# Kernel optimization log

Measured on AMD Instinct MI355X. Metric: run time of the kernel, lower is better.

Reference implementation:

```python
import jax, jax.numpy as jnp
import numpy as np

CHNN = 1024
K = 2048


def _conv1x1(W, b, x):
    # x: (B, C_in, L), W: (C_out, C_in), b: (C_out,)
    return jnp.einsum('oc,bcl->bol', W, x) + b[None, :, None]


def setup_inputs() -> dict:
    key = jax.random.key(0)
    ks = jax.random.split(key, 10)
    s = 0.02
    return {
        'vc': jax.random.normal(ks[0], (1, CHNN, K), dtype=jnp.float32),
        'vm': jax.random.normal(ks[1], (1, CHNN, K), dtype=jnp.float32),
        'W_ak': jax.random.normal(ks[2], (K, CHNN), dtype=jnp.float32) * s,
        'b_ak': jax.random.normal(ks[3], (K,), dtype=jnp.float32) * s,
        'W_c': jax.random.normal(ks[4], (CHNN, CHNN), dtype=jnp.float32) * s,
        'b_c': jax.random.normal(ks[5], (CHNN,), dtype=jnp.float32) * s,
        'W_mad': jax.random.normal(ks[6], (CHNN, CHNN), dtype=jnp.float32) * s,
        'b_mad': jax.random.normal(ks[7], (CHNN,), dtype=jnp.float32) * s,
        'W_gcn': jax.random.normal(ks[8], (CHNN, CHNN), dtype=jnp.float32) * s,
        'b_gcn': jax.random.normal(ks[9], (CHNN,), dtype=jnp.float32) * s,
    }


def reference(vc, vm, W_ak, b_ak, W_c, b_c, W_mad, b_mad, W_gcn, b_gcn):
    # vcw: (1, K, L) assignment logits; softmax over the K (channel) dim
    vcw = _conv1x1(W_ak, b_ak, vc)
    vcw = jax.nn.softmax(vcw, axis=1)
    w = vcw[0].T                      # (L, K)  (batch forced to 1 by squeeze(0))
    # vm features: (1, CHNN, K)
    vmr = jax.nn.relu(_conv1x1(W_c, b_c, vm))
    # F.linear(vm, w): contract last dim (K) with w's second dim -> (1, CHNN, L)
    vma = jnp.einsum('bck,lk->bcl', vmr, w)
    vma = _conv1x1(W_mad, b_mad, vma)  # (1, CHNN, L)
    # dense adjacency over positions: (1, L, L)
    A = jnp.einsum('bck,bcl->bkl', vma, vma)
    # GCN: x (1, K, CHNN) @ W + b, then softmax(A) @ x  (requires L == K)
    x = jnp.swapaxes(vmr, 1, 2) @ W_gcn + b_gcn
    A = jax.nn.softmax(A, axis=-1)
    out = A @ x                        # (1, L, CHNN)
    return jnp.swapaxes(out, 1, 2)     # (1, CHNN, L)
```

## Files before the change

### kernel.cpp

```cpp
#include <hip/hip_runtime.h>
#include <hip/hip_bf16.h>


typedef __bf16 bf16x4 __attribute__((ext_vector_type(4)));
typedef __bf16 bf16x8 __attribute__((ext_vector_type(8)));
typedef float  f32x4  __attribute__((ext_vector_type(4)));

typedef const void __attribute__((address_space(1)))* gptr_t;
typedef void       __attribute__((address_space(3)))* lptr_t;

__device__ __forceinline__ void load16_lds(const __bf16* g, __bf16* l)
{
    __builtin_amdgcn_global_load_lds((gptr_t)g, (lptr_t)l, 16, 0, 0);
}

template<typename OT, int TM_, int TN_, int BIAS_, bool RELU_, int STORE_>
struct GC {
    using OUT_T = OT;
    static constexpr int TM = TM_, TN = TN_, BIAS = BIAS_, STORE = STORE_;
    static constexpr bool RELU = RELU_;
    static constexpr int SMEM = 2 * (TM_ + TN_) * 32 * 2;
};

template<class CF>
__device__ __forceinline__ void gemm_body(
    int bid, char* smem,
    const __bf16* __restrict__ A, const __bf16* __restrict__ B,
    const float* __restrict__ bias,
    typename CF::OUT_T* __restrict__ C, typename CF::OUT_T* __restrict__ CT,
    int M, int N, int K, int ntx)
{
    constexpr int TM = CF::TM, TN = CF::TN;
    constexpr int FM = TM / 32, FN = TN / 32;
    constexpr int NA = TM / 64, NB = TN / 64;
    __bf16* sA = (__bf16*)smem;
    __bf16* sB = (__bf16*)smem + 2 * TM * 32;
    const int tid = threadIdx.x, lane = tid & 63, wv = tid >> 6;
    const int m0 = (bid / ntx) * TM, n0 = (bid % ntx) * TN;
    const int mw = (wv >> 1) * (FM * 16), nw = (wv & 1) * (FN * 16);

    f32x4 acc[FM][FN];
    #pragma unroll
    for (int i = 0; i < FM; ++i)
        #pragma unroll
        for (int j = 0; j < FN; ++j)
            acc[i][j] = (f32x4){0.f, 0.f, 0.f, 0.f};

    const __bf16* gA = A + (size_t)m0 * K;
    const __bf16* gB = B + (size_t)n0 * K;

    auto stage = [&](int k0, int buf) {
        #pragma unroll
        for (int i = 0; i < NA; ++i) {
            const int c = (wv * NA + i) * 64 + lane;
            load16_lds(gA + (size_t)(c >> 2) * K + k0 + (c & 3) * 8,
                       &sA[buf * TM * 32 + (wv * NA + i) * 512]);
        }
        #pragma unroll
        for (int i = 0; i < NB; ++i) {
            const int c = (wv * NB + i) * 64 + lane;
            load16_lds(gB + (size_t)(c >> 2) * K + k0 + (c & 3) * 8,
                       &sB[buf * TN * 32 + (wv * NB + i) * 512]);
        }
    };

    stage(0, 0);
    int cur = 0;
    for (int k0 = 0; k0 < K; k0 += 32) {
        __syncthreads();
        if (k0 + 32 < K) stage(k0 + 32, cur ^ 1);
        bf16x8 af[FM], bfr[FN];
        #pragma unroll
        for (int i = 0; i < FM; ++i)
            af[i] = *(const bf16x8*)&sA[cur * TM * 32 + (mw + i * 16 + (lane & 15)) * 32 + (lane >> 4) * 8];
        #pragma unroll
        for (int j = 0; j < FN; ++j)
            bfr[j] = *(const bf16x8*)&sB[cur * TN * 32 + (nw + j * 16 + (lane & 15)) * 32 + (lane >> 4) * 8];
        #pragma unroll
        for (int i = 0; i < FM; ++i)
            #pragma unroll
            for (int j = 0; j < FN; ++j)
                acc[i][j] = __builtin_amdgcn_mfma_f32_16x16x32_bf16(af[i], bfr[j], acc[i][j], 0, 0, 0);
        cur ^= 1;
    }

    #pragma unroll
    for (int i = 0; i < FM; ++i) {
        const int rowb = m0 + mw + i * 16 + (lane >> 4) * 4;
        #pragma unroll
        for (int j = 0; j < FN; ++j) {
            const int col = n0 + nw + j * 16 + (lane & 15);
            f32x4 v = acc[i][j];
            #pragma unroll
            for (int r = 0; r < 4; ++r) {
                float f = v[r];
                if (CF::BIAS == 1) f += bias[rowb + r];
                if (CF::BIAS == 2) f += bias[col];
                if (CF::RELU) f = fmaxf(f, 0.f);
                v[r] = f;
            }
            if (CF::STORE == 0 || CF::STORE == 2) {
                #pragma unroll
                for (int r = 0; r < 4; ++r)
                    C[(size_t)(rowb + r) * N + col] = (typename CF::OUT_T)v[r];
            }
            if (CF::STORE == 1 || CF::STORE == 2) {
                if constexpr (sizeof(typename CF::OUT_T) == 4) {
                    *(f32x4*)&CT[(size_t)col * M + rowb] = v;
                } else {
                    bf16x4 w = { (__bf16)v[0], (__bf16)v[1], (__bf16)v[2], (__bf16)v[3] };
                    *(bf16x4*)&CT[(size_t)col * M + rowb] = w;
                }
            }
        }
    }
}

template<class CF>
__global__ __launch_bounds__(256, 2)
void gemm1(const __bf16* __restrict__ A, const __bf16* __restrict__ B,
           const float* __restrict__ bias,
           typename CF::OUT_T* __restrict__ C, typename CF::OUT_T* __restrict__ CT,
           int M, int N, int K, int ntx)
{
    __shared__ char smem[CF::SMEM];
    gemm_body<CF>(blockIdx.x, smem, A, B, bias, C, CT, M, N, K, ntx);
}

template<class C1, class C2>
__global__ __launch_bounds__(256, 2)
void gemm2(int nblk1,
           const __bf16* __restrict__ A1, const __bf16* __restrict__ B1,
           const float* __restrict__ b1,
           typename C1::OUT_T* __restrict__ C1p, typename C1::OUT_T* __restrict__ CT1,
           int M1, int N1, int K1, int ntx1,
           const __bf16* __restrict__ A2, const __bf16* __restrict__ B2,
           const float* __restrict__ b2,
           typename C2::OUT_T* __restrict__ C2p, typename C2::OUT_T* __restrict__ CT2,
           int M2, int N2, int K2, int ntx2)
{
    constexpr int S = C1::SMEM > C2::SMEM ? C1::SMEM : C2::SMEM;
    __shared__ char smem[S];
    if ((int)blockIdx.x < nblk1)
        gemm_body<C1>(blockIdx.x, smem, A1, B1, b1, C1p, CT1, M1, N1, K1, ntx1);
    else
        gemm_body<C2>(blockIdx.x - nblk1, smem, A2, B2, b2, C2p, CT2, M2, N2, K2, ntx2);
}

__device__ __forceinline__ void softmax_row(__bf16* __restrict__ p)
{
    __shared__ float red[256];
    const int t = threadIdx.x;
    bf16x8 v = *(bf16x8*)&p[t * 8];
    float f[8];
    float m = -1e30f;
    #pragma unroll
    for (int r = 0; r < 8; ++r) { f[r] = (float)v[r]; m = fmaxf(m, f[r]); }
    red[t] = m;
    __syncthreads();
    for (int s = 128; s > 0; s >>= 1) {
        if (t < s) red[t] = fmaxf(red[t], red[t + s]);
        __syncthreads();
    }
    m = red[0];
    __syncthreads();
    float sum = 0.f;
    #pragma unroll
    for (int r = 0; r < 8; ++r) { f[r] = expf(f[r] - m); sum += f[r]; }
    red[t] = sum;
    __syncthreads();
    for (int s = 128; s > 0; s >>= 1) {
        if (t < s) red[t] += red[t + s];
        __syncthreads();
    }
    const float inv = 1.f / red[0];
    bf16x8 w;
    #pragma unroll
    for (int r = 0; r < 8; ++r) w[r] = (__bf16)(f[r] * inv);
    *(bf16x8*)&p[t * 8] = w;
}

template<class C1, class C2>
__global__ __launch_bounds__(256, 2)
void gemm2sm(int nblk1, int nblk2,
             const __bf16* __restrict__ A1, const __bf16* __restrict__ B1,
             const float* __restrict__ b1,
             typename C1::OUT_T* __restrict__ C1p,
             int M1, int N1, int K1, int ntx1,
             const __bf16* __restrict__ A2, const __bf16* __restrict__ B2,
             const float* __restrict__ b2,
             typename C2::OUT_T* __restrict__ C2p,
             int M2, int N2, int K2, int ntx2,
             __bf16* __restrict__ SM)
{
    constexpr int S = C1::SMEM > C2::SMEM ? C1::SMEM : C2::SMEM;
    __shared__ char smem[S];
    const int b = blockIdx.x;
    if (b < nblk1)
        gemm_body<C1>(b, smem, A1, B1, b1, C1p, (typename C1::OUT_T*)nullptr,
                      M1, N1, K1, ntx1);
    else if (b < nblk1 + nblk2)
        gemm_body<C2>(b - nblk1, smem, A2, B2, b2, C2p, (typename C2::OUT_T*)nullptr,
                      M2, N2, K2, ntx2);
    else
        softmax_row(SM + (size_t)(b - nblk1 - nblk2) * 2048);
}

__device__ __forceinline__ void tp_tile(const float* __restrict__ in,
                                        __bf16* __restrict__ outp,
                                        int R, int C, int bx, int by)
{
    __shared__ float t[32][33];
    const int tx = threadIdx.x & 31, ty = threadIdx.x >> 5;
    #pragma unroll
    for (int i = ty; i < 32; i += 8)
        t[i][tx] = in[(size_t)(by + i) * C + (bx + tx)];
    __syncthreads();
    #pragma unroll
    for (int i = ty; i < 32; i += 8)
        outp[(size_t)(bx + i) * R + (by + tx)] = (__bf16)t[tx][i];
}

__device__ __forceinline__ void cast_blk(const float* __restrict__ s,
                                         __bf16* __restrict__ d, int blk)
{
    const int i = blk * 1024 + threadIdx.x * 4;
    float4 v = *(const float4*)&s[i];
    bf16x4 w = { (__bf16)v.x, (__bf16)v.y, (__bf16)v.z, (__bf16)v.w };
    *(bf16x4*)&d[i] = w;
}

__global__ __launch_bounds__(256)
void prep(const float* __restrict__ vc, __bf16* __restrict__ vcT,
          const float* __restrict__ vm, __bf16* __restrict__ vmT,
          const float* __restrict__ W_ak, __bf16* __restrict__ W_akb,
          const float* __restrict__ W_c, __bf16* __restrict__ W_cb,
          const float* __restrict__ W_mad, __bf16* __restrict__ W_madb,
          const float* __restrict__ W_gcn, __bf16* __restrict__ W_gcnT)
{
    const int x = blockIdx.x;
    if (blockIdx.z == 0) {
        const float* in = (x < 2048) ? vc : vm;
        __bf16* o       = (x < 2048) ? vcT : vmT;
        const int e = x & 2047;
        tp_tile(in, o, 1024, 2048, (e & 63) * 32, (e >> 6) * 32);
    } else if (blockIdx.z == 1) {
        if (x < 2048)      cast_blk(W_ak, W_akb, x);
        else if (x < 3072) cast_blk(W_c, W_cb, x - 2048);
        else               cast_blk(W_mad, W_madb, x - 3072);
    } else {
        if (x >= 1024) return;
        tp_tile(W_gcn, W_gcnT, 1024, 1024, (x & 31) * 32, (x >> 5) * 32);
    }
}

__global__ __launch_bounds__(256)
void row_softmax_k(__bf16* __restrict__ A)
{
    softmax_row(A + (size_t)blockIdx.x * 2048);
}

extern "C" void kernel_launch(void* const* d_in, const int* in_sizes, int n_in,
                              void* d_out, int out_size, void* d_ws, size_t ws_size,
                              hipStream_t stream)
{
    const float* vc    = (const float*)d_in[0];
    const float* vm    = (const float*)d_in[1];
    const float* W_ak  = (const float*)d_in[2];
    const float* b_ak  = (const float*)d_in[3];
    const float* W_c   = (const float*)d_in[4];
    const float* b_c   = (const float*)d_in[5];
    const float* W_mad = (const float*)d_in[6];
    const float* b_mad = (const float*)d_in[7];
    const float* W_gcn = (const float*)d_in[8];
    const float* b_gcn = (const float*)d_in[9];
    float* out = (float*)d_out;

    char* ws = (char*)d_ws;
    const size_t MB = 1u << 20;
    __bf16* ST     = (__bf16*)(ws);
    __bf16* P      = (__bf16*)(ws);
    __bf16* vcT    = (__bf16*)(ws + 8 * MB);
    __bf16* vmaT   = (__bf16*)(ws + 8 * MB);
    __bf16* W_akb  = (__bf16*)(ws + 12 * MB);
    __bf16* vmm    = (__bf16*)(ws + 12 * MB);
    __bf16* vmT    = (__bf16*)(ws + 16 * MB);
    __bf16* xT     = (__bf16*)(ws + 16 * MB);
    __bf16* W_cb   = (__bf16*)(ws + 20 * MB);
    __bf16* W_madb = (__bf16*)(ws + 22 * MB);
    __bf16* vmrT   = (__bf16*)(ws + 24 * MB);
    __bf16* W_gcnT = (__bf16*)(ws + 28 * MB);

    using G3  = GC<__bf16, 128, 64, 2, false, 0>;
    using G5  = GC<__bf16, 128, 64, 1, true,  1>;
    using G6  = GC<__bf16, 128, 64, 0, false, 0>;
    using G11 = GC<__bf16, 128, 64, 1, false, 0>;
    using G7  = GC<__bf16, 64,  64, 2, false, 0>;
    using G9  = GC<__bf16, 128, 64, 0, false, 0>;
    using G12 = GC<float,  64,  64, 0, false, 1>;

    prep<<<dim3(4096, 1, 3), 256, 0, stream>>>(vc, vcT, vm, vmT, W_ak, W_akb,
                                               W_c, W_cb, W_mad, W_madb,
                                               W_gcn, W_gcnT);
    gemm2<G3, G5><<<768, 256, 0, stream>>>(512,
        vcT, W_akb, b_ak, ST, (__bf16*)nullptr, 2048, 2048, 1024, 32,
        W_cb, vmT, b_c, (__bf16*)nullptr, vmrT, 1024, 2048, 1024, 32);
    gemm2sm<G6, G11><<<2560, 256, 0, stream>>>(256, 256,
        W_madb, vmrT, nullptr, vmm, 1024, 2048, 1024, 32,
        W_gcnT, vmrT, b_gcn, xT, 1024, 2048, 1024, 32,
        ST);
    gemm1<G7><<<512, 256, 0, stream>>>(ST, vmm, b_mad, vmaT, (__bf16*)nullptr,
                                       2048, 1024, 2048, 16);
    gemm1<G9><<<512, 256, 0, stream>>>(vmaT, vmaT, nullptr, P, (__bf16*)nullptr,
                                       2048, 2048, 1024, 32);
    row_softmax_k<<<2048, 256, 0, stream>>>(P);
    gemm1<G12><<<512, 256, 0, stream>>>(P, xT, nullptr, (float*)nullptr, out,
                                        2048, 1024, 2048, 16);
}
```

Baseline: 211.3 us.

## Switch GEMMs and softmax to single-wave blocks with barrier-free waitcnt pipelining

Reworks every GEMM into a 64-thread block that owns a 64x64 tile. Because there is only one wave, __syncthreads is replaced by s_waitcnt on vmcnt, and the direct-to-LDS loads are double-buffered with a prefetch distance of two stages. Row softmax is rewritten to use one wave and shuffle reductions, removing the LDS tree reduction and barriers. The cost is more blocks, less operand reuse across waves, and reliance on hand-coded waitcnt encodings being correct for LDS-bound async loads.

Result: no change. 208.2 us (-1.4%).

```diff
diff --git a/kernel.cpp b/kernel.cpp
--- a/kernel.cpp
+++ b/kernel.cpp
@@ -14,82 +14,91 @@
     __builtin_amdgcn_global_load_lds((gptr_t)g, (lptr_t)l, 16, 0, 0);
 }
 
-template<typename OT, int TM_, int TN_, int BIAS_, bool RELU_, int STORE_>
+#define WAITCNT_VM8 0x0F78
+#define WAITCNT_VM0 0x0F70
+
+template<typename OT, int BIAS_, bool RELU_, int STORE_>
 struct GC {
     using OUT_T = OT;
-    static constexpr int TM = TM_, TN = TN_, BIAS = BIAS_, STORE = STORE_;
+    static constexpr int BIAS = BIAS_, STORE = STORE_;
     static constexpr bool RELU = RELU_;
-    static constexpr int SMEM = 2 * (TM_ + TN_) * 32 * 2;
 };
 
 template<class CF>
 __device__ __forceinline__ void gemm_body(
-    int bid, char* smem,
+    int bid, __bf16* sA, __bf16* sB,
     const __bf16* __restrict__ A, const __bf16* __restrict__ B,
     const float* __restrict__ bias,
     typename CF::OUT_T* __restrict__ C, typename CF::OUT_T* __restrict__ CT,
     int M, int N, int K, int ntx)
 {
-    constexpr int TM = CF::TM, TN = CF::TN;
-    constexpr int FM = TM / 32, FN = TN / 32;
-    constexpr int NA = TM / 64, NB = TN / 64;
-    __bf16* sA = (__bf16*)smem;
-    __bf16* sB = (__bf16*)smem + 2 * TM * 32;
-    const int tid = threadIdx.x, lane = tid & 63, wv = tid >> 6;
-    const int m0 = (bid / ntx) * TM, n0 = (bid % ntx) * TN;
-    const int mw = (wv >> 1) * (FM * 16), nw = (wv & 1) * (FN * 16);
-
-    f32x4 acc[FM][FN];
-    #pragma unroll
-    for (int i = 0; i < FM; ++i)
-        #pragma unroll
-        for (int j = 0; j < FN; ++j)
-            acc[i][j] = (f32x4){0.f, 0.f, 0.f, 0.f};
-
+    const int lane = threadIdx.x & 63;
+    const int m0 = (bid / ntx) * 64, n0 = (bid % ntx) * 64;
     const __bf16* gA = A + (size_t)m0 * K;
     const __bf16* gB = B + (size_t)n0 * K;
 
+    f32x4 acc[4][4];
+    #pragma unroll
+    for (int i = 0; i < 4; ++i)
+        #pragma unroll
+        for (int j = 0; j < 4; ++j)
+            acc[i][j] = (f32x4){0.f, 0.f, 0.f, 0.f};
+
     auto stage = [&](int k0, int buf) {
         #pragma unroll
-        for (int i = 0; i < NA; ++i) {
-            const int c = (wv * NA + i) * 64 + lane;
+        for (int i = 0; i < 4; ++i) {
+            const int c = i * 64 + lane;
             load16_lds(gA + (size_t)(c >> 2) * K + k0 + (c & 3) * 8,
-                       &sA[buf * TM * 32 + (wv * NA + i) * 512]);
-        }
-        #pragma unroll
-        for (int i = 0; i < NB; ++i) {
-            const int c = (wv * NB + i) * 64 + lane;
+                       &sA[buf * 2048 + i * 512]);
+        }
+        #pragma unroll
+        for (int i = 0; i < 4; ++i) {
+            const int c = i * 64 + lane;
             load16_lds(gB + (size_t)(c >> 2) * K + k0 + (c & 3) * 8,
-                       &sB[buf * TN * 32 + (wv * NB + i) * 512]);
+                       &sB[buf * 2048 + i * 512]);
         }
     };
 
     stage(0, 0);
+    stage(32, 1);
     int cur = 0;
-    for (int k0 = 0; k0 < K; k0 += 32) {
-        __syncthreads();
-        if (k0 + 32 < K) stage(k0 + 32, cur ^ 1);
-        bf16x8 af[FM], bfr[FN];
-        #pragma unroll
-        for (int i = 0; i < FM; ++i)
-            af[i] = *(const bf16x8*)&sA[cur * TM * 32 + (mw + i * 16 + (lane & 15)) * 32 + (lane >> 4) * 8];
-        #pragma unroll
-        for (int j = 0; j < FN; ++j)
-            bfr[j] = *(const bf16x8*)&sB[cur * TN * 32 + (nw + j * 16 + (lane & 15)) * 32 + (lane >> 4) * 8];
-        #pragma unroll
-        for (int i = 0; i < FM; ++i)
+    for (int k0 = 0; k0 < K - 32; k0 += 32) {
+        __builtin_amdgcn_s_waitcnt(WAITCNT_VM8);
+        bf16x8 af[4], bfr[4];
+        #pragma unroll
+        for (int i = 0; i < 4; ++i) {
+            af[i]  = *(const bf16x8*)&sA[cur * 2048 + (i * 16 + (lane & 15)) * 32 + (lane >> 4) * 8];
+            bfr[i] = *(const bf16x8*)&sB[cur * 2048 + (i * 16 + (lane & 15)) * 32 + (lane >> 4) * 8];
+        }
+        #pragma unroll
+        for (int i = 0; i < 4; ++i)
             #pragma unroll
-            for (int j = 0; j < FN; ++j)
+            for (int j = 0; j < 4; ++j)
                 acc[i][j] = __builtin_amdgcn_mfma_f32_16x16x32_bf16(af[i], bfr[j], acc[i][j], 0, 0, 0);
+        if (k0 + 64 < K) stage(k0 + 64, cur);
         cur ^= 1;
     }
-
-    #pragma unroll
-    for (int i = 0; i < FM; ++i) {
-        const int rowb = m0 + mw + i * 16 + (lane >> 4) * 4;
-        #pragma unroll
-        for (int j = 0; j < FN; ++j) {
-            const int col = n0 + nw + j * 16 + (lane & 15);
+    __builtin_amdgcn_s_waitcnt(WAITCNT_VM0);
+    {
+        bf16x8 af[4], bfr[4];
+        #pragma unroll
+        for (int i = 0; i < 4; ++i) {
+            af[i]  = *(const bf16x8*)&sA[cur * 2048 + (i * 16 + (lane & 15)) * 32 + (lane >> 4) * 8];
+            bfr[i] = *(const bf16x8*)&sB[cur * 2048 + (i * 16 + (lane & 15)) * 32 + (lane >> 4) * 8];
+        }
+        #pragma unroll
+        for (int i = 0; i < 4; ++i)
+            #pragma unroll
+            for (int j = 0; j < 4; ++j)
+                acc[i][j] = __builtin_amdgcn_mfma_f32_16x16x32_bf16(af[i], bfr[j], acc[i][j], 0, 0, 0);
+    }
+
+    #pragma unroll
+    for (int i = 0; i < 4; ++i) {
+        const int rowb = m0 + i * 16 + (lane >> 4) * 4;
+        #pragma unroll
+        for (int j = 0; j < 4; ++j) {
+            const int col = n0 + j * 16 + (lane & 15);
             f32x4 v = acc[i][j];
             #pragma unroll
             for (int r = 0; r < 4; ++r) {
@@ -99,12 +108,11 @@
                 if (CF::RELU) f = fmaxf(f, 0.f);
                 v[r] = f;
             }
-            if (CF::STORE == 0 || CF::STORE == 2) {
+            if (CF::STORE == 0) {
                 #pragma unroll
                 for (int r = 0; r < 4; ++r)
                     C[(size_t)(rowb + r) * N + col] = (typename CF::OUT_T)v[r];
-            }
-            if (CF::STORE == 1 || CF::STORE == 2) {
+            } else {
                 if constexpr (sizeof(typename CF::OUT_T) == 4) {
                     *(f32x4*)&CT[(size_t)col * M + rowb] = v;
                 } else {
@@ -116,94 +124,97 @@
     }
 }
 
+__device__ __forceinline__ void softmax_row_w(__bf16* __restrict__ p)
+{
+    const int lane = threadIdx.x & 63;
+    bf16x8 v[4];
+    float f[32];
+    #pragma unroll
+    for (int r = 0; r < 4; ++r)
+        v[r] = *(const bf16x8*)&p[(r * 64 + lane) * 8];
+    float m = -1e30f;
+    #pragma unroll
+    for (int r = 0; r < 4; ++r)
+        #pragma unroll
+        for (int j = 0; j < 8; ++j) {
+            f[r * 8 + j] = (float)v[r][j];
+            m = fmaxf(m, f[r * 8 + j]);
+        }
+    #pragma unroll
+    for (int s = 1; s < 64; s <<= 1) m = fmaxf(m, __shfl_xor(m, s, 64));
+    float sum = 0.f;
+    #pragma unroll
+    for (int i = 0; i < 32; ++i) { f[i] = expf(f[i] - m); sum += f[i]; }
+    #pragma unroll
+    for (int s = 1; s < 64; s <<= 1) sum += __shfl_xor(sum, s, 64);
+    const float inv = 1.f / sum;
+    #pragma unroll
+    for (int r = 0; r < 4; ++r) {
+        bf16x8 w;
+        #pragma unroll
+        for (int j = 0; j < 8; ++j) w[j] = (__bf16)(f[r * 8 + j] * inv);
+        *(bf16x8*)&p[(r * 64 + lane) * 8] = w;
+    }
+}
+
 template<class CF>
-__global__ __launch_bounds__(256, 2)
-void gemm1(const __bf16* __restrict__ A, const __bf16* __restrict__ B,
-           const float* __restrict__ bias,
-           typename CF::OUT_T* __restrict__ C, typename CF::OUT_T* __restrict__ CT,
-           int M, int N, int K, int ntx)
-{
-    __shared__ char smem[CF::SMEM];
-    gemm_body<CF>(blockIdx.x, smem, A, B, bias, C, CT, M, N, K, ntx);
+__global__ __launch_bounds__(64, 2)
+void gemm1w(const __bf16* __restrict__ A, const __bf16* __restrict__ B,
+            const float* __restrict__ bias,
+            typename CF::OUT_T* __restrict__ C, typename CF::OUT_T* __restrict__ CT,
+            int M, int N, int K, int ntx)
+{
+    __shared__ __bf16 sAB[8192];
+    gemm_body<CF>(blockIdx.x, sAB, sAB + 4096, A, B, bias, C, CT, M, N, K, ntx);
 }
 
 template<class C1, class C2>
-__global__ __launch_bounds__(256, 2)
-void gemm2(int nblk1,
-           const __bf16* __restrict__ A1, const __bf16* __restrict__ B1,
-           const float* __restrict__ b1,
-           typename C1::OUT_T* __restrict__ C1p, typename C1::OUT_T* __restrict__ CT1,
-           int M1, int N1, int K1, int ntx1,
-           const __bf16* __restrict__ A2, const __bf16* __restrict__ B2,
-           const float* __restrict__ b2,
-           typename C2::OUT_T* __restrict__ C2p, typename C2::OUT_T* __restrict__ CT2,
-           int M2, int N2, int K2, int ntx2)
-{
-    constexpr int S = C1::SMEM > C2::SMEM ? C1::SMEM : C2::SMEM;
-    __shared__ char smem[S];
-    if ((int)blockIdx.x < nblk1)
-        gemm_body<C1>(blockIdx.x, smem, A1, B1, b1, C1p, CT1, M1, N1, K1, ntx1);
-    else
-        gemm_body<C2>(blockIdx.x - nblk1, smem, A2, B2, b2, C2p, CT2, M2, N2, K2, ntx2);
-}
-
-__device__ __forceinline__ void softmax_row(__bf16* __restrict__ p)
-{
-    __shared__ float red[256];
-    const int t = threadIdx.x;
-    bf16x8 v = *(bf16x8*)&p[t * 8];
-    float f[8];
-    float m = -1e30f;
-    #pragma unroll
-    for (int r = 0; r < 8; ++r) { f[r] = (float)v[r]; m = fmaxf(m, f[r]); }
-    red[t] = m;
-    __syncthreads();
-    for (int s = 128; s > 0; s >>= 1) {
-        if (t < s) red[t] = fmaxf(red[t], red[t + s]);
-        __syncthreads();
-    }
-    m = red[0];
-    __syncthreads();
-    float sum = 0.f;
-    #pragma unroll
-    for (int r = 0; r < 8; ++r) { f[r] = expf(f[r] - m); sum += f[r]; }
-    red[t] = sum;
-    __syncthreads();
-    for (int s = 128; s > 0; s >>= 1) {
-        if (t < s) red[t] += red[t + s];
-        __syncthreads();
-    }
-    const float inv = 1.f / red[0];
-    bf16x8 w;
-    #pragma unroll
-    for (int r = 0; r < 8; ++r) w[r] = (__bf16)(f[r] * inv);
-    *(bf16x8*)&p[t * 8] = w;
-}
-
-template<class C1, class C2>
-__global__ __launch_bounds__(256, 2)
-void gemm2sm(int nblk1, int nblk2,
-             const __bf16* __restrict__ A1, const __bf16* __restrict__ B1,
-             const float* __restrict__ b1,
-             typename C1::OUT_T* __restrict__ C1p,
-             int M1, int N1, int K1, int ntx1,
-             const __bf16* __restrict__ A2, const __bf16* __restrict__ B2,
-             const float* __restrict__ b2,
-             typename C2::OUT_T* __restrict__ C2p,
-             int M2, int N2, int K2, int ntx2,
-             __bf16* __restrict__ SM)
-{
-    constexpr int S = C1::SMEM > C2::SMEM ? C1::SMEM : C2::SMEM;
-    __shared__ char smem[S];
+__global__ __launch_bounds__(64, 2)
+void gemm2w(int nblk1,
+            const __bf16* __restrict__ A1, const __bf16* __restrict__ B1,
+            const float* __restrict__ b1,
+            typename C1::OUT_T* __restrict__ C1p, typename C1::OUT_T* __restrict__ CT1,
+            int M1, int N1, int K1, int ntx1,
+            const __bf16* __restrict__ A2, const __bf16* __restrict__ B2,
+            const float* __restrict__ b2,
+            typename C2::OUT_T* __restrict__ C2p, typename C2::OUT_T* __restrict__ CT2,
+            int M2, int N2, int K2, int ntx2)
+{
+    __shared__ __bf16 sAB[8192];
     const int b = blockIdx.x;
     if (b < nblk1)
-        gemm_body<C1>(b, smem, A1, B1, b1, C1p, (typename C1::OUT_T*)nullptr,
-                      M1, N1, K1, ntx1);
+        gemm_body<C1>(b, sAB, sAB + 4096, A1, B1, b1, C1p, CT1, M1, N1, K1, ntx1);
+    else
+        gemm_body<C2>(b - nblk1, sAB, sAB + 4096, A2, B2, b2, C2p, CT2, M2, N2, K2, ntx2);
+}
+
+template<class C1, class C2>
+__global__ __launch_bounds__(64, 2)
+void gemm2smw(int nblk1, int nblk2,
+              const __bf16* __restrict__ A1, const __bf16* __restrict__ B1,
+              const float* __restrict__ b1, typename C1::OUT_T* __restrict__ C1p,
+              int M1, int N1, int K1, int ntx1,
+              const __bf16* __restrict__ A2, const __bf16* __restrict__ B2,
+              const float* __restrict__ b2, typename C2::OUT_T* __restrict__ C2p,
+              int M2, int N2, int K2, int ntx2,
+              __bf16* __restrict__ SM)
+{
+    __shared__ __bf16 sAB[8192];
+    const int b = blockIdx.x;
+    if (b < nblk1)
+        gemm_body<C1>(b, sAB, sAB + 4096, A1, B1, b1, C1p,
+                      (typename C1::OUT_T*)nullptr, M1, N1, K1, ntx1);
     else if (b < nblk1 + nblk2)
-        gemm_body<C2>(b - nblk1, smem, A2, B2, b2, C2p, (typename C2::OUT_T*)nullptr,
-                      M2, N2, K2, ntx2);
+        gemm_body<C2>(b - nblk1, sAB, sAB + 4096, A2, B2, b2, C2p,
+                      (typename C2::OUT_T*)nullptr, M2, N2, K2, ntx2);
     else
-        softmax_row(SM + (size_t)(b - nblk1 - nblk2) * 2048);
+        softmax_row_w(SM + (size_t)(b - nblk1 - nblk2) * 2048);
+}
+
+__global__ __launch_bounds__(64)
+void row_softmax_w(__bf16* __restrict__ A)
+{
+    softmax_row_w(A + (size_t)blockIdx.x * 2048);
 }
 
 __device__ __forceinline__ void tp_tile(const float* __restrict__ in,
@@ -252,12 +263,6 @@
         if (x >= 1024) return;
         tp_tile(W_gcn, W_gcnT, 1024, 1024, (x & 31) * 32, (x >> 5) * 32);
     }
-}
-
-__global__ __launch_bounds__(256)
-void row_softmax_k(__bf16* __restrict__ A)
-{
-    softmax_row(A + (size_t)blockIdx.x * 2048);
 }
 
 extern "C" void kernel_launch(void* const* d_in, const int* in_sizes, int n_in,
@@ -291,29 +296,29 @@
     __bf16* vmrT   = (__bf16*)(ws + 24 * MB);
     __bf16* W_gcnT = (__bf16*)(ws + 28 * MB);
 
-    using G3  = GC<__bf16, 128, 64, 2, false, 0>;
-    using G5  = GC<__bf16, 128, 64, 1, true,  1>;
-    using G6  = GC<__bf16, 128, 64, 0, false, 0>;
-    using G11 = GC<__bf16, 128, 64, 1, false, 0>;
-    using G7  = GC<__bf16, 64,  64, 2, false, 0>;
-    using G9  = GC<__bf16, 128, 64, 0, false, 0>;
-    using G12 = GC<float,  64,  64, 0, false, 1>;
+    using G3  = GC<__bf16, 2, false, 0>;
+    using G5  = GC<__bf16, 1, true,  1>;
+    using G6  = GC<__bf16, 0, false, 0>;
+    using G11 = GC<__bf16, 1, false, 0>;
+    using G7  = GC<__bf16, 2, false, 0>;
+    using G9  = GC<__bf16, 0, false, 0>;
+    using G12 = GC<float,  0, false, 1>;
 
     prep<<<dim3(4096, 1, 3), 256, 0, stream>>>(vc, vcT, vm, vmT, W_ak, W_akb,
                                                W_c, W_cb, W_mad, W_madb,
                                                W_gcn, W_gcnT);
-    gemm2<G3, G5><<<768, 256, 0, stream>>>(512,
+    gemm2w<G3, G5><<<1536, 64, 0, stream>>>(1024,
         vcT, W_akb, b_ak, ST, (__bf16*)nullptr, 2048, 2048, 1024, 32,
         W_cb, vmT, b_c, (__bf16*)nullptr, vmrT, 1024, 2048, 1024, 32);
-    gemm2sm<G6, G11><<<2560, 256, 0, stream>>>(256, 256,
+    gemm2smw<G6, G11><<<3072, 64, 0, stream>>>(512, 512,
         W_madb, vmrT, nullptr, vmm, 1024, 2048, 1024, 32,
         W_gcnT, vmrT, b_gcn, xT, 1024, 2048, 1024, 32,
         ST);
-    gemm1<G7><<<512, 256, 0, stream>>>(ST, vmm, b_mad, vmaT, (__bf16*)nullptr,
+    gemm1w<G7><<<512, 64, 0, stream>>>(ST, vmm, b_mad, vmaT, (__bf16*)nullptr,
                                        2048, 1024, 2048, 16);
-    gemm1<G9><<<512, 256, 0, stream>>>(vmaT, vmaT, nullptr, P, (__bf16*)nullptr,
-                                       2048, 2048, 1024, 32);
-    row_softmax_k<<<2048, 256, 0, stream>>>(P);
-    gemm1<G12><<<512, 256, 0, stream>>>(P, xT, nullptr, (float*)nullptr, out,
+    gemm1w<G9><<<1024, 64, 0, stream>>>(vmaT, vmaT, nullptr, P, (__bf16*)nullptr,
+                                        2048, 2048, 1024, 32);
+    row_softmax_w<<<2048, 64, 0, stream>>>(P);
+    gemm1w<G12><<<512, 64, 0, stream>>>(P, xT, nullptr, (float*)nullptr, out,
                                         2048, 1024, 2048, 16);
 }
```
